# Kernel optimization log

Measured on AMD Instinct MI355X. Metric: run time of the kernel, lower is better.

The kernel has to match this reference:

```python
import jax, jax.numpy as jnp
import numpy as np

DIM_MODEL = 1024
NUM_HEADS = 16
HEAD_DIM = DIM_MODEL // NUM_HEADS
NEG = -1000000000.0


def setup_inputs() -> dict:
    key = jax.random.key(0)
    ks = jax.random.split(key, 11)
    B, S, D = 2, 2048, DIM_MODEL
    s = 1.0 / np.sqrt(D)
    return {
        "q": jax.random.normal(ks[0], (B, S, D), jnp.float32),
        "k": jax.random.normal(ks[1], (B, S, D), jnp.float32),
        "v": jax.random.normal(ks[2], (B, S, D), jnp.float32),
        "Wq": jax.random.normal(ks[3], (D, D), jnp.float32) * s,
        "bq": jnp.zeros((D,), jnp.float32),
        "Wk": jax.random.normal(ks[4], (D, D), jnp.float32) * s,
        "bk": jnp.zeros((D,), jnp.float32),
        "Wv": jax.random.normal(ks[5], (D, D), jnp.float32) * s,
        "bv": jnp.zeros((D,), jnp.float32),
        "Wo": jax.random.normal(ks[6], (D, D), jnp.float32) * s,
        "bo": jnp.zeros((D,), jnp.float32),
    }


def reference(q, k, v, Wq, bq, Wk, bk, Wv, bv, Wo, bo):
    B, S, D = q.shape
    H, hd = NUM_HEADS, HEAD_DIM

    def proj(x, W, b):
        # torch Linear: x @ W.T + b, then split heads -> [B, H, S, hd]
        y = jnp.einsum("bsd,ed->bse", x, W) + b
        return y.reshape(B, S, H, hd).transpose(0, 2, 1, 3)

    qh = proj(q, Wq, bq)
    kh = proj(k, Wk, bk)
    vh = proj(v, Wv, bv)

    scores = jnp.einsum("bhqd,bhkd->bhqk", qh, kh) / np.sqrt(hd)
    # torch.triu(ones(S,S), diagonal=0): upper triangle INCLUDING diagonal is masked
    mask = jnp.triu(jnp.ones((S, S), bool))
    scores = jnp.where(mask, NEG, scores)
    # softmax over dim=-2 (query axis), as in the original module
    attn = jax.nn.softmax(scores, axis=-2)
    ctx = jnp.einsum("bhqk,bhkd->bhqd", attn, vh)  # [B,H,S,hd]
    ctx = ctx.transpose(0, 2, 1, 3).reshape(B, S, D)
    return jnp.einsum("bsd,ed->bse", ctx, Wo) + bo
```

## Files before the change

### kernel.cpp

```cpp
#include <hip/hip_runtime.h>

typedef __bf16 bf16;
typedef __attribute__((ext_vector_type(8))) __bf16 bf16x8;
typedef __attribute__((ext_vector_type(2))) __bf16 bf16x2;
typedef __attribute__((ext_vector_type(4))) float f32x4;

#define AS1 __attribute__((address_space(1)))
#define AS3 __attribute__((address_space(3)))

#define BB 2
#define SS 2048
#define DD 1024
#define HH 16
#define HD 64
#define BH (BB*HH)

#define QSCALE 0.1803368801111244f

static __device__ __forceinline__ f32x4 mfma16(bf16x8 a, bf16x8 b, f32x4 c) {
  return __builtin_amdgcn_mfma_f32_16x16x32_bf16(a, b, c, 0, 0, 0);
}
static __device__ __forceinline__ float fexp2(float x) {
  return __builtin_amdgcn_exp2f(x);
}

static __device__ __forceinline__ void swz1024(int bid, int& bh, int& a, int& b2) {
  int c = bid & 7, j = bid >> 3;
  bh = c + 8 * (j & 3);
  int rem = j >> 2;
  a = rem & 15;
  b2 = rem >> 4;
}

__global__ __launch_bounds__(256) void cvt_w(const float* __restrict__ s0, const float* __restrict__ s1,
                                             const float* __restrict__ s2, const float* __restrict__ s3,
                                             bf16* __restrict__ o0, bf16* __restrict__ o1,
                                             bf16* __restrict__ o2, bf16* __restrict__ o3) {
  const int z = blockIdx.y;
  const float* s = (z == 0) ? s0 : (z == 1) ? s1 : (z == 2) ? s2 : s3;
  bf16* o = (z == 0) ? o0 : (z == 1) ? o1 : (z == 2) ? o2 : o3;
  int i = blockIdx.x * 256 + threadIdx.x;
  const float4* sp = (const float4*)s;
  float4 a = sp[2 * i], b = sp[2 * i + 1];
  bf16x8 v;
  v[0] = (bf16)a.x; v[1] = (bf16)a.y; v[2] = (bf16)a.z; v[3] = (bf16)a.w;
  v[4] = (bf16)b.x; v[5] = (bf16)b.y; v[6] = (bf16)b.z; v[7] = (bf16)b.w;
  ((bf16x8*)o)[i] = v;
}

__global__ __launch_bounds__(256) void cvt_x(const float* __restrict__ s0, const float* __restrict__ s1,
                                             const float* __restrict__ s2,
                                             bf16* __restrict__ o0, bf16* __restrict__ o1,
                                             bf16* __restrict__ o2) {
  const int z = blockIdx.y;
  const float* s = (z == 0) ? s0 : (z == 1) ? s1 : s2;
  bf16* o = (z == 0) ? o0 : (z == 1) ? o1 : o2;
  int i = blockIdx.x * 256 + threadIdx.x;
  const float4* sp = (const float4*)s;
  float4 a = sp[2 * i], b = sp[2 * i + 1];
  bf16x8 v;
  v[0] = (bf16)a.x; v[1] = (bf16)a.y; v[2] = (bf16)a.z; v[3] = (bf16)a.w;
  v[4] = (bf16)b.x; v[5] = (bf16)b.y; v[6] = (bf16)b.z; v[7] = (bf16)b.w;
  ((bf16x8*)o)[i] = v;
}

__device__ __forceinline__ void gemm_core(const bf16* __restrict__ A,
                                          const bf16* __restrict__ Bm, int K,
                                          int m0, int n0, int w, int l,
                                          bf16* sA, bf16* sB, f32x4 (&acc)[4][4]) {
  const int l15 = l & 15, lg = l >> 4;
  const int wr = (w >> 1) * 64, wc = (w & 1) * 64;
  const int fv = (l15 >> 1) & 3;
  for (int kt = 0; kt < K; kt += 32) {
#pragma unroll
    for (int i = 0; i < 2; ++i) {
      int t = i * 256 + w * 64 + l;
      const int r = t >> 2, cs = (t & 3) ^ ((r >> 1) & 3);
      const bf16* ga = A + (size_t)(m0 + r) * K + kt + cs * 8;
      const bf16* gb = Bm + (size_t)(n0 + r) * K + kt + cs * 8;
      __builtin_amdgcn_global_load_lds((const AS1 void*)ga,
                                       (AS3 void*)(sA + (i * 256 + w * 64) * 8), 16, 0, 0);
      __builtin_amdgcn_global_load_lds((const AS1 void*)gb,
                                       (AS3 void*)(sB + (i * 256 + w * 64) * 8), 16, 0, 0);
    }
    __syncthreads();
    bf16x8 af[4], bfr[4];
#pragma unroll
    for (int m = 0; m < 4; ++m)
      af[m] = *(const bf16x8*)(sA + (wr + m * 16 + l15) * 32 + (lg ^ fv) * 8);
#pragma unroll
    for (int n = 0; n < 4; ++n)
      bfr[n] = *(const bf16x8*)(sB + (wc + n * 16 + l15) * 32 + (lg ^ fv) * 8);
#pragma unroll
    for (int m = 0; m < 4; ++m)
#pragma unroll
      for (int n = 0; n < 4; ++n)
        acc[m][n] = mfma16(af[m], bfr[n], acc[m][n]);
    __syncthreads();
  }
}

__global__ __launch_bounds__(256) void proj_gemm(
    const bf16* __restrict__ Xq, const bf16* __restrict__ Xk, const bf16* __restrict__ Xv,
    const bf16* __restrict__ Wq, const bf16* __restrict__ Wk, const bf16* __restrict__ Wv,
    const float* __restrict__ bq, const float* __restrict__ bk, const float* __restrict__ bv,
    bf16* __restrict__ Oq, bf16* __restrict__ Ok, bf16* __restrict__ Ovt) {
  __shared__ __align__(16) bf16 sA[128 * 32];
  __shared__ __align__(16) bf16 sB[128 * 32];
  const int bid = blockIdx.x;
  const int c = bid & 7, u = bid >> 3;
  const int mt = c * 4 + (u & 3);
  const int nt = (u >> 2) & 7;
  const int z = u >> 5;
  const bf16* A = (z == 0) ? Xq : ((z == 1) ? Xk : Xv);
  const bf16* W = (z == 0) ? Wq : ((z == 1) ? Wk : Wv);
  const float* bias = (z == 0) ? bq : ((z == 1) ? bk : bv);
  const int tid = threadIdx.x, l = tid & 63, w = tid >> 6;
  const int m0 = mt * 128, n0 = nt * 128;
  f32x4 acc[4][4] = {};
  gemm_core(A, W, DD, m0, n0, w, l, sA, sB, acc);
  const int l15 = l & 15, lg = l >> 4;
  const int wr = (w >> 1) * 64, wc = (w & 1) * 64;
#pragma unroll
  for (int n = 0; n < 4; ++n) {
    int col = n0 + wc + n * 16 + l15;
    float bb = bias[col];
    int h = col >> 6, d = col & 63;
#pragma unroll
    for (int m = 0; m < 4; ++m) {
#pragma unroll
      for (int r = 0; r < 4; ++r) {
        int row = m0 + wr + m * 16 + lg * 4 + r;
        int b = row >> 11, s = row & (SS - 1);
        float vv = acc[m][n][r] + bb;
        if (z == 0) vv *= QSCALE;
        if (z != 2)
          ((z == 0) ? Oq : Ok)[(((size_t)(b * HH + h)) * SS + s) * HD + d] = (bf16)vv;
        else
          Ovt[(size_t)(b * HH + h) * SS * HD + ((s >> 5) * 64 + d) * 32 + (s & 31)] = (bf16)vv;
      }
    }
  }
}

__global__ __launch_bounds__(256) void out_gemm(const bf16* __restrict__ A,
                                                const bf16* __restrict__ W,
                                                const float* __restrict__ bias,
                                                float* __restrict__ out) {
  __shared__ __align__(16) bf16 sA[128 * 32];
  __shared__ __align__(16) bf16 sB[128 * 32];
  const int bid = blockIdx.x;
  const int c = bid & 7, u = bid >> 3;
  const int mt = c * 4 + (u & 3);
  const int nt = (u >> 2) & 7;
  const int tid = threadIdx.x, l = tid & 63, w = tid >> 6;
  const int m0 = mt * 128, n0 = nt * 128;
  f32x4 acc[4][4] = {};
  gemm_core(A, W, DD, m0, n0, w, l, sA, sB, acc);
  const int l15 = l & 15, lg = l >> 4;
  const int wr = (w >> 1) * 64, wc = (w & 1) * 64;
#pragma unroll
  for (int n = 0; n < 4; ++n) {
    int col = n0 + wc + n * 16 + l15;
    float bb = bias[col];
#pragma unroll
    for (int m = 0; m < 4; ++m)
#pragma unroll
      for (int r = 0; r < 4; ++r) {
        int row = m0 + wr + m * 16 + lg * 4 + r;
        out[(size_t)row * DD + col] = acc[m][n][r] + bb;
      }
  }
}

__global__ __launch_bounds__(256) void colz(const bf16* __restrict__ Qb,
                                            const bf16* __restrict__ Kb,
                                            float* __restrict__ zPart) {
  __shared__ float zred[4][64];
  int bh, pair, qh;
  swz1024(blockIdx.x, bh, pair, qh);
  const int tid = threadIdx.x, l = tid & 63, w = tid >> 6;
  const int l15 = l & 15, lg = l >> 4;
  const bf16* Q = Qb + (size_t)bh * SS * HD;
  const bf16* Kh = Kb + (size_t)bh * SS * HD;

  for (int half = 0; half < 2; ++half) {
    const int s = half ? (31 - pair) : pair;
    const int c0 = s * 64;
    bf16x8 kf[4][2];
#pragma unroll
    for (int kt = 0; kt < 4; ++kt) {
      kf[kt][0] = *(const bf16x8*)&Kh[(c0 + kt * 16 + l15) * HD + lg * 8];
      kf[kt][1] = *(const bf16x8*)&Kh[(c0 + kt * 16 + l15) * HD + 32 + lg * 8];
    }
    float z[4] = {};
    const int qstart = c0 + qh * 64 + w * 16;
    bf16x8 qa0, qa1, qn0, qn1;
    if (qstart < SS) {
      qa0 = *(const bf16x8*)&Q[(qstart + l15) * HD + lg * 8];
      qa1 = *(const bf16x8*)&Q[(qstart + l15) * HD + 32 + lg * 8];
    }
    for (int qb = qstart; qb < SS; qb += 128) {
      const int qnext = qb + 128;
      if (qnext < SS) {
        qn0 = *(const bf16x8*)&Q[(qnext + l15) * HD + lg * 8];
        qn1 = *(const bf16x8*)&Q[(qnext + l15) * HD + 32 + lg * 8];
      }
      f32x4 d[4] = {};
#pragma unroll
      for (int kt = 0; kt < 4; ++kt) {
        d[kt] = mfma16(qa0, kf[kt][0], d[kt]);
        d[kt] = mfma16(qa1, kf[kt][1], d[kt]);
      }
#pragma unroll
      for (int kt = 0; kt < 4; ++kt) {
        const int kcol = c0 + kt * 16 + l15;
#pragma unroll
        for (int r = 0; r < 4; ++r) {
          int qq = qb + lg * 4 + r;
          z[kt] += (qq > kcol) ? fexp2(d[kt][r]) : 0.f;
        }
      }
      qa0 = qn0; qa1 = qn1;
    }
#pragma unroll
    for (int kt = 0; kt < 4; ++kt) {
      z[kt] += __shfl_xor(z[kt], 16);
      z[kt] += __shfl_xor(z[kt], 32);
    }
    if (l < 16) {
#pragma unroll
      for (int kt = 0; kt < 4; ++kt) zred[w][kt * 16 + l15] = z[kt];
    }
    __syncthreads();
    if (tid < 64) {
      float zs = zred[0][tid] + zred[1][tid] + zred[2][tid] + zred[3][tid];
      zPart[((size_t)qh * BH + bh) * SS + c0 + tid] = zs;
    }
    __syncthreads();
  }
}

__global__ __launch_bounds__(256) void rzfin(const float* __restrict__ zPart,
                                             float* __restrict__ cRZ) {
  int i = blockIdx.x * 256 + threadIdx.x;
  f32x4 a = ((const f32x4*)zPart)[i];
  f32x4 b = ((const f32x4*)(zPart + (size_t)BH * SS))[i];
  f32x4 r;
#pragma unroll
  for (int j = 0; j < 4; ++j) {
    float s = a[j] + b[j];
    r[j] = (s > 0.f) ? 1.0f / s : 0.f;
  }
  ((f32x4*)cRZ)[i] = r;
}

__global__ __launch_bounds__(256) void vscale(bf16* __restrict__ Vt,
                                              const float* __restrict__ cRZ,
                                              float* __restrict__ vlastB) {
  int i = blockIdx.x * 256 + threadIdx.x;
  int ks8 = i & 3;
  int d = (i >> 2) & 63;
  int ts = (i >> 8) & 63;
  int bh = i >> 14;
  bf16* p = Vt + ((((size_t)bh * 64 + ts) * 64 + d) * 32) + ks8 * 8;
  const float* rz = cRZ + (size_t)bh * SS + ts * 32 + ks8 * 8;
  bf16x8 v = *(const bf16x8*)p;
  if (ts == 63 && ks8 == 3) vlastB[bh * 64 + d] = (float)v[7] * (1.0f / (float)SS);
  f32x4 r0 = *(const f32x4*)rz, r1 = *(const f32x4*)(rz + 4);
  bf16x8 o;
#pragma unroll
  for (int j = 0; j < 4; ++j) o[j] = (bf16)((float)v[j] * r0[j]);
#pragma unroll
  for (int j = 0; j < 4; ++j) o[4 + j] = (bf16)((float)v[4 + j] * r1[j]);
  *(bf16x8*)p = o;
}

template <bool DIAG>
static __device__ __forceinline__ void chunk_compute(
    const bf16* sKe, const bf16* sVe, int k0, int qw,
    const bf16x8 (&qa)[2][2], f32x4 (&acc)[2][4], int l15, int lg) {
  const int fv = (l15 >> 1) & 3;
  const int slK = (lg ^ fv) * 8;
  bf16x8 kf00 = *(const bf16x8*)(sKe + l15 * 32 + slK);
  bf16x8 kf01 = *(const bf16x8*)(sKe + 1024 + l15 * 32 + slK);
  bf16x8 kf10 = *(const bf16x8*)(sKe + (16 + l15) * 32 + slK);
  bf16x8 kf11 = *(const bf16x8*)(sKe + 1024 + (16 + l15) * 32 + slK);
  union U { unsigned int u[4]; bf16x8 v; };
  U vf[4];
#pragma unroll
  for (int dt = 0; dt < 4; ++dt) {
    const bf16* base = sVe + (dt * 16 + l15) * 32;
    uint2 lo = *(const uint2*)&base[((lg >> 1) ^ fv) * 8 + (lg & 1) * 4];
    uint2 hi = *(const uint2*)&base[(((lg >> 1) + 2) ^ fv) * 8 + (lg & 1) * 4];
    vf[dt].u[0] = lo.x; vf[dt].u[1] = lo.y; vf[dt].u[2] = hi.x; vf[dt].u[3] = hi.y;
  }
  const int kb0i = k0 + lg * 4, kb1i = k0 + 16 + lg * 4;
#pragma unroll
  for (int qt = 0; qt < 2; ++qt) {
    f32x4 s0 = {}, s1 = {};
    s0 = mfma16(kf00, qa[qt][0], s0);
    s0 = mfma16(kf01, qa[qt][1], s0);
    s1 = mfma16(kf10, qa[qt][0], s1);
    s1 = mfma16(kf11, qa[qt][1], s1);
    const int qq = qw + qt * 16 + l15;
    U pa;
#pragma unroll
    for (int hw = 0; hw < 2; ++hw) {
      bf16x2 t0, t1;
#pragma unroll
      for (int r = 0; r < 2; ++r) {
        int rr = hw * 2 + r;
        float p0 = fexp2(s0[rr]);
        float p1 = fexp2(s1[rr]);
        if (DIAG) {
          p0 = (kb0i + rr < qq) ? p0 : 0.f;
          p1 = (kb1i + rr < qq) ? p1 : 0.f;
        }
        t0[r] = (bf16)p0;
        t1[r] = (bf16)p1;
      }
      pa.u[hw] = __builtin_bit_cast(unsigned int, t0);
      pa.u[hw + 2] = __builtin_bit_cast(unsigned int, t1);
    }
#pragma unroll
    for (int dt = 0; dt < 4; ++dt)
      acc[qt][dt] = mfma16(pa.v, vf[dt].v, acc[qt][dt]);
  }
}

__global__ __launch_bounds__(256, 2) void attn_ctx(const bf16* __restrict__ Qb,
                                                   const bf16* __restrict__ Kb,
                                                   const bf16* __restrict__ Vt,
                                                   bf16* __restrict__ P0,
                                                   bf16* __restrict__ P1,
                                                   bf16* __restrict__ P2,
                                                   bf16* __restrict__ P3) {
  __shared__ __align__(16) bf16 sK[2 * 32 * 32];
  __shared__ __align__(16) bf16 sV[64 * 32];
  int bh, a, b2;
  swz1024(blockIdx.x, bh, a, b2);
  const int pr = a & 7;
  const int j = (b2 << 1) | (a >> 3);
  const int tid = threadIdx.x, l = tid & 63, w = tid >> 6;
  const int l15 = l & 15, lg = l >> 4;
  const bf16* Q = Qb + (size_t)bh * SS * HD;
  const bf16* Kh = Kb + (size_t)bh * SS * HD;
  const bf16* V = Vt + (size_t)bh * SS * HD;
  bf16* ctxP = (j == 0) ? P0 : (j == 1) ? P1 : (j == 2) ? P2 : P3;
  const int b = bh >> 4, h = bh & 15;

  const int skk = tid >> 7, sr = (tid >> 2) & 31, sc = tid & 3;
  const int scs = sc ^ ((sr >> 1) & 3);
  const int vr = tid >> 2;
  const int vcs = (tid & 3) ^ ((vr >> 1) & 3);
  bf16* dK = sK + (size_t)w * 512;
  bf16* dV = sV + (size_t)w * 512;

  for (int half = 0; half < 2; ++half) {
    const int T = half ? (15 - pr) : pr;
    const int q0 = T * 128;
    const int qw = q0 + w * 32;

    bf16x8 qa[2][2];
#pragma unroll
    for (int qt = 0; qt < 2; ++qt)
#pragma unroll
      for (int kk = 0; kk < 2; ++kk)
        qa[qt][kk] = *(const bf16x8*)&Q[(qw + qt * 16 + l15) * HD + kk * 32 + lg * 8];

    f32x4 acc[2][4] = {};
    const int kend = q0 + 128;
    for (int k0 = j * 32; k0 < kend; k0 += 128) {
      const bf16* gK = Kh + (size_t)(k0 + sr) * HD + skk * 32 + scs * 8;
      const bf16* gV = V + (((size_t)(k0 >> 5)) << 11) + vr * 32 + vcs * 8;
      __builtin_amdgcn_global_load_lds((const AS1 void*)gK, (AS3 void*)dK, 16, 0, 0);
      __builtin_amdgcn_global_load_lds((const AS1 void*)gV, (AS3 void*)dV, 16, 0, 0);
      __syncthreads();
      if (k0 < qw)
        chunk_compute<false>(sK, sV, k0, qw, qa, acc, l15, lg);
      else if (k0 == qw)
        chunk_compute<true>(sK, sV, k0, qw, qa, acc, l15, lg);
      __syncthreads();
    }

#pragma unroll
    for (int qt = 0; qt < 2; ++qt)
#pragma unroll
      for (int r = 0; r < 4; ++r) {
        int q = qw + qt * 16 + lg * 4 + r;
#pragma unroll
        for (int dt = 0; dt < 4; ++dt)
          ctxP[((size_t)(b * SS + q)) * DD + h * HD + dt * 16 + l15] =
              (bf16)acc[qt][dt][r];
      }
  }
}

__global__ __launch_bounds__(256) void ctxfin(const bf16* __restrict__ P1,
                                              const bf16* __restrict__ P2,
                                              const bf16* __restrict__ P3,
                                              const float* __restrict__ vlastB,
                                              bf16* __restrict__ ctx) {
  int i = blockIdx.x * 256 + threadIdx.x;
  int e0 = i * 8;
  int row = e0 >> 10, col = e0 & (DD - 1);
  int b = row >> 11;
  int vidx = (b * HH + (col >> 6)) * 64 + (col & 63);
  bf16x8 p0 = ((const bf16x8*)ctx)[i];
  bf16x8 p1 = ((const bf16x8*)P1)[i];
  bf16x8 p2 = ((const bf16x8*)P2)[i];
  bf16x8 p3 = ((const bf16x8*)P3)[i];
  f32x4 v0 = *(const f32x4*)&vlastB[vidx];
  f32x4 v1 = *(const f32x4*)&vlastB[vidx + 4];
  bf16x8 o;
#pragma unroll
  for (int jj = 0; jj < 4; ++jj)
    o[jj] = (bf16)(((float)p0[jj] + (float)p1[jj]) + ((float)p2[jj] + (float)p3[jj]) + v0[jj]);
#pragma unroll
  for (int jj = 0; jj < 4; ++jj)
    o[4 + jj] = (bf16)(((float)p0[4 + jj] + (float)p1[4 + jj]) +
                       ((float)p2[4 + jj] + (float)p3[4 + jj]) + v1[jj]);
  ((bf16x8*)ctx)[i] = o;
}

extern "C" void kernel_launch(void* const* d_in, const int* in_sizes, int n_in,
                              void* d_out, int out_size, void* d_ws, size_t ws_size,
                              hipStream_t stream) {
  const float* q  = (const float*)d_in[0];
  const float* k  = (const float*)d_in[1];
  const float* v  = (const float*)d_in[2];
  const float* Wq = (const float*)d_in[3];
  const float* bq = (const float*)d_in[4];
  const float* Wk = (const float*)d_in[5];
  const float* bk = (const float*)d_in[6];
  const float* Wv = (const float*)d_in[7];
  const float* bv = (const float*)d_in[8];
  const float* Wo = (const float*)d_in[9];
  const float* bo = (const float*)d_in[10];

  char* ws = (char*)d_ws;
  const size_t SZP = (size_t)4096 * 1024 * 2;
  const size_t SZW = (size_t)1024 * 1024 * 2;
  bf16* Qb   = (bf16*)(ws + 0 * SZP);
  bf16* Kb   = (bf16*)(ws + 1 * SZP);
  bf16* Vt   = (bf16*)(ws + 2 * SZP);
  bf16* ctxb = (bf16*)(ws + 3 * SZP);
  bf16* qb16 = (bf16*)(ws + 4 * SZP);
  bf16* kb16 = (bf16*)(ws + 5 * SZP);
  bf16* vb16 = (bf16*)(ws + 6 * SZP);
  bf16* Wqb  = (bf16*)(ws + 7 * SZP + 0 * SZW);
  bf16* Wkb  = (bf16*)(ws + 7 * SZP + 1 * SZW);
  bf16* Wvb  = (bf16*)(ws + 7 * SZP + 2 * SZW);
  bf16* Wob  = (bf16*)(ws + 7 * SZP + 3 * SZW);
  float* zPart = (float*)(ws + 7 * SZP + 4 * SZW);
  float* cRZ   = zPart + (size_t)2 * BH * SS;
  float* vlastB = cRZ + (size_t)BH * SS;

  cvt_w<<<dim3(512, 4), 256, 0, stream>>>(Wq, Wk, Wv, Wo, Wqb, Wkb, Wvb, Wob);
  cvt_x<<<dim3(2048, 3), 256, 0, stream>>>(q, k, v, qb16, kb16, vb16);

  proj_gemm<<<768, 256, 0, stream>>>(
      qb16, kb16, vb16, Wqb, Wkb, Wvb, bq, bk, bv, Qb, Kb, Vt);

  colz<<<1024, 256, 0, stream>>>(Qb, Kb, zPart);
  rzfin<<<(BH * SS / 4) / 256, 256, 0, stream>>>(zPart, cRZ);
  vscale<<<(BH * HD * SS / 8) / 256, 256, 0, stream>>>(Vt, cRZ, vlastB);
  attn_ctx<<<1024, 256, 0, stream>>>(Qb, Kb, Vt, ctxb, qb16, kb16, vb16);
  ctxfin<<<(4096 * 1024 / 8) / 256, 256, 0, stream>>>(qb16, kb16, vb16, vlastB, ctxb);

  out_gemm<<<256, 256, 0, stream>>>(ctxb, Wob, bo, (float*)d_out);
}
```

Baseline: 147.5 us.

## Fuse input bf16 conversion and context partial reduction into GEMM tile loads

Removes the separate fp32-to-bf16 activation conversion kernel by converting inside the projection GEMM's A-tile load. It also removes the context finalisation kernel by summing the four partial contexts plus the V-last term while loading A tiles in the output GEMM. This is meant to save two launches and the full-tensor write and read of intermediate buffers. In exchange, the A loads become synchronous register loads instead of async global-to-LDS copies, and each A element is re-read in fp32 or as four partials for every column tile.

```diff
diff --git a/kernel.cpp b/kernel.cpp
--- a/kernel.cpp
+++ b/kernel.cpp
@@ -48,60 +48,8 @@
   ((bf16x8*)o)[i] = v;
 }
 
-__global__ __launch_bounds__(256) void cvt_x(const float* __restrict__ s0, const float* __restrict__ s1,
-                                             const float* __restrict__ s2,
-                                             bf16* __restrict__ o0, bf16* __restrict__ o1,
-                                             bf16* __restrict__ o2) {
-  const int z = blockIdx.y;
-  const float* s = (z == 0) ? s0 : (z == 1) ? s1 : s2;
-  bf16* o = (z == 0) ? o0 : (z == 1) ? o1 : o2;
-  int i = blockIdx.x * 256 + threadIdx.x;
-  const float4* sp = (const float4*)s;
-  float4 a = sp[2 * i], b = sp[2 * i + 1];
-  bf16x8 v;
-  v[0] = (bf16)a.x; v[1] = (bf16)a.y; v[2] = (bf16)a.z; v[3] = (bf16)a.w;
-  v[4] = (bf16)b.x; v[5] = (bf16)b.y; v[6] = (bf16)b.z; v[7] = (bf16)b.w;
-  ((bf16x8*)o)[i] = v;
-}
-
-__device__ __forceinline__ void gemm_core(const bf16* __restrict__ A,
-                                          const bf16* __restrict__ Bm, int K,
-                                          int m0, int n0, int w, int l,
-                                          bf16* sA, bf16* sB, f32x4 (&acc)[4][4]) {
-  const int l15 = l & 15, lg = l >> 4;
-  const int wr = (w >> 1) * 64, wc = (w & 1) * 64;
-  const int fv = (l15 >> 1) & 3;
-  for (int kt = 0; kt < K; kt += 32) {
-#pragma unroll
-    for (int i = 0; i < 2; ++i) {
-      int t = i * 256 + w * 64 + l;
-      const int r = t >> 2, cs = (t & 3) ^ ((r >> 1) & 3);
-      const bf16* ga = A + (size_t)(m0 + r) * K + kt + cs * 8;
-      const bf16* gb = Bm + (size_t)(n0 + r) * K + kt + cs * 8;
-      __builtin_amdgcn_global_load_lds((const AS1 void*)ga,
-                                       (AS3 void*)(sA + (i * 256 + w * 64) * 8), 16, 0, 0);
-      __builtin_amdgcn_global_load_lds((const AS1 void*)gb,
-                                       (AS3 void*)(sB + (i * 256 + w * 64) * 8), 16, 0, 0);
-    }
-    __syncthreads();
-    bf16x8 af[4], bfr[4];
-#pragma unroll
-    for (int m = 0; m < 4; ++m)
-      af[m] = *(const bf16x8*)(sA + (wr + m * 16 + l15) * 32 + (lg ^ fv) * 8);
-#pragma unroll
-    for (int n = 0; n < 4; ++n)
-      bfr[n] = *(const bf16x8*)(sB + (wc + n * 16 + l15) * 32 + (lg ^ fv) * 8);
-#pragma unroll
-    for (int m = 0; m < 4; ++m)
-#pragma unroll
-      for (int n = 0; n < 4; ++n)
-        acc[m][n] = mfma16(af[m], bfr[n], acc[m][n]);
-    __syncthreads();
-  }
-}
-
 __global__ __launch_bounds__(256) void proj_gemm(
-    const bf16* __restrict__ Xq, const bf16* __restrict__ Xk, const bf16* __restrict__ Xv,
+    const float* __restrict__ Xq, const float* __restrict__ Xk, const float* __restrict__ Xv,
     const bf16* __restrict__ Wq, const bf16* __restrict__ Wk, const bf16* __restrict__ Wv,
     const float* __restrict__ bq, const float* __restrict__ bk, const float* __restrict__ bv,
     bf16* __restrict__ Oq, bf16* __restrict__ Ok, bf16* __restrict__ Ovt) {
@@ -112,15 +60,46 @@
   const int mt = c * 4 + (u & 3);
   const int nt = (u >> 2) & 7;
   const int z = u >> 5;
-  const bf16* A = (z == 0) ? Xq : ((z == 1) ? Xk : Xv);
+  const float* X = (z == 0) ? Xq : ((z == 1) ? Xk : Xv);
   const bf16* W = (z == 0) ? Wq : ((z == 1) ? Wk : Wv);
   const float* bias = (z == 0) ? bq : ((z == 1) ? bk : bv);
   const int tid = threadIdx.x, l = tid & 63, w = tid >> 6;
   const int m0 = mt * 128, n0 = nt * 128;
-  f32x4 acc[4][4] = {};
-  gemm_core(A, W, DD, m0, n0, w, l, sA, sB, acc);
   const int l15 = l & 15, lg = l >> 4;
   const int wr = (w >> 1) * 64, wc = (w & 1) * 64;
+  const int fv = (l15 >> 1) & 3;
+  f32x4 acc[4][4] = {};
+  for (int kt = 0; kt < DD; kt += 32) {
+#pragma unroll
+    for (int i = 0; i < 2; ++i) {
+      int t = i * 256 + tid;
+      int r = t >> 2, cs = (t & 3) ^ ((r >> 1) & 3);
+      const bf16* gb = W + (size_t)(n0 + r) * DD + kt + cs * 8;
+      __builtin_amdgcn_global_load_lds((const AS1 void*)gb,
+                                       (AS3 void*)(sB + (i * 256 + w * 64) * 8), 16, 0, 0);
+      const float* gx = X + (size_t)(m0 + r) * DD + kt + cs * 8;
+      float4 x0 = *(const float4*)gx;
+      float4 x1 = *(const float4*)(gx + 4);
+      bf16x8 o;
+      o[0] = (bf16)x0.x; o[1] = (bf16)x0.y; o[2] = (bf16)x0.z; o[3] = (bf16)x0.w;
+      o[4] = (bf16)x1.x; o[5] = (bf16)x1.y; o[6] = (bf16)x1.z; o[7] = (bf16)x1.w;
+      *(bf16x8*)(sA + t * 8) = o;
+    }
+    __syncthreads();
+    bf16x8 af[4], bfr[4];
+#pragma unroll
+    for (int m = 0; m < 4; ++m)
+      af[m] = *(const bf16x8*)(sA + (wr + m * 16 + l15) * 32 + (lg ^ fv) * 8);
+#pragma unroll
+    for (int n = 0; n < 4; ++n)
+      bfr[n] = *(const bf16x8*)(sB + (wc + n * 16 + l15) * 32 + (lg ^ fv) * 8);
+#pragma unroll
+    for (int m = 0; m < 4; ++m)
+#pragma unroll
+      for (int n = 0; n < 4; ++n)
+        acc[m][n] = mfma16(af[m], bfr[n], acc[m][n]);
+    __syncthreads();
+  }
 #pragma unroll
   for (int n = 0; n < 4; ++n) {
     int col = n0 + wc + n * 16 + l15;
@@ -143,7 +122,11 @@
   }
 }
 
-__global__ __launch_bounds__(256) void out_gemm(const bf16* __restrict__ A,
+__global__ __launch_bounds__(256) void out_gemm(const bf16* __restrict__ P0,
+                                                const bf16* __restrict__ P1,
+                                                const bf16* __restrict__ P2,
+                                                const bf16* __restrict__ P3,
+                                                const float* __restrict__ vlastB,
                                                 const bf16* __restrict__ W,
                                                 const float* __restrict__ bias,
                                                 float* __restrict__ out) {
@@ -155,10 +138,51 @@
   const int nt = (u >> 2) & 7;
   const int tid = threadIdx.x, l = tid & 63, w = tid >> 6;
   const int m0 = mt * 128, n0 = nt * 128;
-  f32x4 acc[4][4] = {};
-  gemm_core(A, W, DD, m0, n0, w, l, sA, sB, acc);
   const int l15 = l & 15, lg = l >> 4;
   const int wr = (w >> 1) * 64, wc = (w & 1) * 64;
+  const int fv = (l15 >> 1) & 3;
+  f32x4 acc[4][4] = {};
+  for (int kt = 0; kt < DD; kt += 32) {
+#pragma unroll
+    for (int i = 0; i < 2; ++i) {
+      int t = i * 256 + tid;
+      int r = t >> 2, cs = (t & 3) ^ ((r >> 1) & 3);
+      const bf16* gb = W + (size_t)(n0 + r) * DD + kt + cs * 8;
+      __builtin_amdgcn_global_load_lds((const AS1 void*)gb,
+                                       (AS3 void*)(sB + (i * 256 + w * 64) * 8), 16, 0, 0);
+      size_t aoff = (size_t)(m0 + r) * DD + kt + cs * 8;
+      bf16x8 p0 = *(const bf16x8*)(P0 + aoff);
+      bf16x8 p1 = *(const bf16x8*)(P1 + aoff);
+      bf16x8 p2 = *(const bf16x8*)(P2 + aoff);
+      bf16x8 p3 = *(const bf16x8*)(P3 + aoff);
+      const float* vl = vlastB + ((m0 + r) >> 11) * DD + kt + cs * 8;
+      f32x4 v0 = *(const f32x4*)vl;
+      f32x4 v1 = *(const f32x4*)(vl + 4);
+      bf16x8 o;
+#pragma unroll
+      for (int j = 0; j < 4; ++j)
+        o[j] = (bf16)(((float)p0[j] + (float)p1[j]) + ((float)p2[j] + (float)p3[j]) + v0[j]);
+#pragma unroll
+      for (int j = 0; j < 4; ++j)
+        o[4 + j] = (bf16)(((float)p0[4 + j] + (float)p1[4 + j]) +
+                          ((float)p2[4 + j] + (float)p3[4 + j]) + v1[j]);
+      *(bf16x8*)(sA + t * 8) = o;
+    }
+    __syncthreads();
+    bf16x8 af[4], bfr[4];
+#pragma unroll
+    for (int m = 0; m < 4; ++m)
+      af[m] = *(const bf16x8*)(sA + (wr + m * 16 + l15) * 32 + (lg ^ fv) * 8);
+#pragma unroll
+    for (int n = 0; n < 4; ++n)
+      bfr[n] = *(const bf16x8*)(sB + (wc + n * 16 + l15) * 32 + (lg ^ fv) * 8);
+#pragma unroll
+    for (int m = 0; m < 4; ++m)
+#pragma unroll
+      for (int n = 0; n < 4; ++n)
+        acc[m][n] = mfma16(af[m], bfr[n], acc[m][n]);
+    __syncthreads();
+  }
 #pragma unroll
   for (int n = 0; n < 4; ++n) {
     int col = n0 + wc + n * 16 + l15;
@@ -397,33 +421,6 @@
   }
 }
 
-__global__ __launch_bounds__(256) void ctxfin(const bf16* __restrict__ P1,
-                                              const bf16* __restrict__ P2,
-                                              const bf16* __restrict__ P3,
-                                              const float* __restrict__ vlastB,
-                                              bf16* __restrict__ ctx) {
-  int i = blockIdx.x * 256 + threadIdx.x;
-  int e0 = i * 8;
-  int row = e0 >> 10, col = e0 & (DD - 1);
-  int b = row >> 11;
-  int vidx = (b * HH + (col >> 6)) * 64 + (col & 63);
-  bf16x8 p0 = ((const bf16x8*)ctx)[i];
-  bf16x8 p1 = ((const bf16x8*)P1)[i];
-  bf16x8 p2 = ((const bf16x8*)P2)[i];
-  bf16x8 p3 = ((const bf16x8*)P3)[i];
-  f32x4 v0 = *(const f32x4*)&vlastB[vidx];
-  f32x4 v1 = *(const f32x4*)&vlastB[vidx + 4];
-  bf16x8 o;
-#pragma unroll
-  for (int jj = 0; jj < 4; ++jj)
-    o[jj] = (bf16)(((float)p0[jj] + (float)p1[jj]) + ((float)p2[jj] + (float)p3[jj]) + v0[jj]);
-#pragma unroll
-  for (int jj = 0; jj < 4; ++jj)
-    o[4 + jj] = (bf16)(((float)p0[4 + jj] + (float)p1[4 + jj]) +
-                       ((float)p2[4 + jj] + (float)p3[4 + jj]) + v1[jj]);
-  ((bf16x8*)ctx)[i] = o;
-}
-
 extern "C" void kernel_launch(void* const* d_in, const int* in_sizes, int n_in,
                               void* d_out, int out_size, void* d_ws, size_t ws_size,
                               hipStream_t stream) {
@@ -445,10 +442,10 @@
   bf16* Qb   = (bf16*)(ws + 0 * SZP);
   bf16* Kb   = (bf16*)(ws + 1 * SZP);
   bf16* Vt   = (bf16*)(ws + 2 * SZP);
-  bf16* ctxb = (bf16*)(ws + 3 * SZP);
-  bf16* qb16 = (bf16*)(ws + 4 * SZP);
-  bf16* kb16 = (bf16*)(ws + 5 * SZP);
-  bf16* vb16 = (bf16*)(ws + 6 * SZP);
+  bf16* ctxP0 = (bf16*)(ws + 3 * SZP);
+  bf16* ctxP1 = (bf16*)(ws + 4 * SZP);
+  bf16* ctxP2 = (bf16*)(ws + 5 * SZP);
+  bf16* ctxP3 = (bf16*)(ws + 6 * SZP);
   bf16* Wqb  = (bf16*)(ws + 7 * SZP + 0 * SZW);
   bf16* Wkb  = (bf16*)(ws + 7 * SZP + 1 * SZW);
   bf16* Wvb  = (bf16*)(ws + 7 * SZP + 2 * SZW);
@@ -458,16 +455,15 @@
   float* vlastB = cRZ + (size_t)BH * SS;
 
   cvt_w<<<dim3(512, 4), 256, 0, stream>>>(Wq, Wk, Wv, Wo, Wqb, Wkb, Wvb, Wob);
-  cvt_x<<<dim3(2048, 3), 256, 0, stream>>>(q, k, v, qb16, kb16, vb16);
 
   proj_gemm<<<768, 256, 0, stream>>>(
-      qb16, kb16, vb16, Wqb, Wkb, Wvb, bq, bk, bv, Qb, Kb, Vt);
+      q, k, v, Wqb, Wkb, Wvb, bq, bk, bv, Qb, Kb, Vt);
 
   colz<<<1024, 256, 0, stream>>>(Qb, Kb, zPart);
   rzfin<<<(BH * SS / 4) / 256, 256, 0, stream>>>(zPart, cRZ);
   vscale<<<(BH * HD * SS / 8) / 256, 256, 0, stream>>>(Vt, cRZ, vlastB);
-  attn_ctx<<<1024, 256, 0, stream>>>(Qb, Kb, Vt, ctxb, qb16, kb16, vb16);
-  ctxfin<<<(4096 * 1024 / 8) / 256, 256, 0, stream>>>(qb16, kb16, vb16, vlastB, ctxb);
-
-  out_gemm<<<256, 256, 0, stream>>>(ctxb, Wob, bo, (float*)d_out);
-}
+  attn_ctx<<<1024, 256, 0, stream>>>(Qb, Kb, Vt, ctxP0, ctxP1, ctxP2, ctxP3);
+
+  out_gemm<<<256, 256, 0, stream>>>(ctxP0, ctxP1, ctxP2, ctxP3, vlastB, Wob, bo,
+                                    (float*)d_out);
+}
```

After: 166.5 us. +12.9%, slower.
